# Optimization experiments

Hardware: AMD Instinct MI355X
Metric: run time of the kernel (lower is better)

## Reference

```python
import jax, jax.numpy as jnp
import numpy as np

SQRT_QKV_DIM = 8.0  # sqrt(qkv_dim=64)


def setup_inputs() -> dict:
    key = jax.random.key(0)
    ks = jax.random.split(key, 8)
    B, H, T, M, d, hid = 4, 16, 512, 512, 64, 16
    return {
        "q": jax.random.normal(ks[0], (B, H, T, d), dtype=jnp.float32),
        "k": jax.random.normal(ks[1], (B, H, M, d), dtype=jnp.float32),
        "v": jax.random.normal(ks[2], (B, H, M, d), dtype=jnp.float32),
        "D_TM": jax.random.uniform(ks[3], (B, T, M), dtype=jnp.float32),
        "mix1_weight": jax.random.uniform(ks[4], (H, 2, hid), minval=-0.7071, maxval=0.7071, dtype=jnp.float32),
        "mix1_bias": jax.random.uniform(ks[5], (H, hid), minval=-0.7071, maxval=0.7071, dtype=jnp.float32),
        "mix2_weight": jax.random.uniform(ks[6], (H, hid, 1), minval=-0.25, maxval=0.25, dtype=jnp.float32),
        "mix2_bias": jax.random.uniform(ks[7], (H, 1), minval=-0.25, maxval=0.25, dtype=jnp.float32),
    }


def reference(q, k, v, D_TM, mix1_weight, mix1_bias, mix2_weight, mix2_bias):
    B, H, T, d = q.shape
    Mc = k.shape[2]
    # scaled dot-product score: (B,H,T,M)
    dot_score = jnp.einsum("bhtd,bhmd->bhtm", q, k) / SQRT_QKV_DIM
    # per-head 2->hidden->1 MLP mixing dot score and distance bias.
    # Avoid explicit stack: linear layer over the 2 score channels expands as
    # dot*W1[:,0,:] + D*W1[:,1,:].  ms1: (B,H,T,M,hid)
    w1_dot = mix1_weight[:, 0, :][None, :, None, None, :]   # (1,H,1,1,hid)
    w1_dist = mix1_weight[:, 1, :][None, :, None, None, :]
    ms1 = (dot_score[..., None] * w1_dot
           + D_TM[:, None, :, :, None] * w1_dist
           + mix1_bias[None, :, None, None, :])
    ms1 = jax.nn.relu(ms1)
    # hidden -> 1: mixed_scores (B,H,T,M)
    mixed = jnp.einsum("bhtmc,hc->bhtm", ms1, mix2_weight[:, :, 0])
    mixed = mixed + mix2_bias[:, 0][None, :, None, None]
    weights = jax.nn.softmax(mixed, axis=3)
    out = jnp.einsum("bhtm,bhmd->bhtd", weights, v)   # (B,H,T,d)
    return out.transpose(0, 2, 1, 3).reshape(B, T, H * d)
```

## Files before the change

### kernel.cpp

```cpp
#include <hip/hip_runtime.h>
#include <stdint.h>

typedef __attribute__((ext_vector_type(8))) short short8;
typedef __attribute__((ext_vector_type(4))) float floatx4;

#define MFMA(a, b, c) __builtin_amdgcn_mfma_f32_16x16x32_bf16(a, b, c, 0, 0, 0)

union Frag { uint32_t u[4]; short8 s; };

__device__ __forceinline__ void packsplit(float a, float b, uint32_t& hi, uint32_t& lo) {
    uint32_t ua = __float_as_uint(a), ub = __float_as_uint(b);
    uint32_t ha = ua & 0xFFFF0000u, hb = ub & 0xFFFF0000u;
    float ra = a - __uint_as_float(ha);
    float rb = b - __uint_as_float(hb);
    hi = (ha >> 16) | hb;
    lo = (__float_as_uint(ra) >> 16) | (__float_as_uint(rb) & 0xFFFF0000u);
}

__device__ __forceinline__ float fexp2(float x) {
#if __has_builtin(__builtin_amdgcn_exp2f)
    return __builtin_amdgcn_exp2f(x);
#else
    return exp2f(x);
#endif
}

#define PHIo 9216
#define PLOo 11520

__global__ __launch_bounds__(256, 2)
void msmha_mfma(const float* __restrict__ qg, const float* __restrict__ kg,
                const float* __restrict__ vg, const float* __restrict__ Dg,
                const float* __restrict__ m1w, const float* __restrict__ m1b,
                const float* __restrict__ m2w, const float* __restrict__ m2b,
                float* __restrict__ outg) {
    __shared__ __align__(16) uint32_t sm[13824];
    __shared__ __align__(16) float4 wlds[16];

    const int tid  = threadIdx.x;
    const int w    = tid >> 6;
    const int lane = tid & 63;
    const int col  = lane & 15;
    const int quad = lane >> 4;

    const int bid = blockIdx.x;
    const int wgT = bid & 7;
    const int bh  = bid >> 3;
    const int h   = bh & 15;
    const int b   = bh >> 4;
    const int t0g = wgT * 64;

    const size_t base = (size_t)bh * 512 * 64;
    const float LOG2E = 1.4426950408889634f;

    if (tid < 16) {
        const float w1d = m1w[h * 32 + tid];
        const float w1s = m1w[h * 32 + 16 + tid];
        const float b1  = m1b[h * 16 + tid];
        const float w2  = m2w[h * 16 + tid];
        wlds[tid] = make_float4(w1d * (0.125f * LOG2E), w1s * LOG2E, b1 * LOG2E, 0.5f * w2);
    }

    float sA = 0.f, sB = 0.f, sC = 0.f;
#pragma unroll 1
    for (int c = 0; c < 16; ++c) {
        const float w2 = m2w[h * 16 + c];
        sA = fmaf(w2, m1w[h * 32 + c], sA);
        sB = fmaf(w2, m1w[h * 32 + 16 + c], sB);
        sC = fmaf(w2, m1b[h * 16 + c], sC);
    }
    const float Ac = sA * (0.0625f * LOG2E);
    const float Bc = sB * (0.5f * LOG2E);
    const float Cc = fmaf(0.5f, sC, m2b[h]) * LOG2E;

    Frag qh[2], ql[2];
    {
        const float* qrow = qg + base + (size_t)(t0g + w * 16 + col) * 64;
#pragma unroll
        for (int ks = 0; ks < 2; ++ks) {
            const float4 f0 = *(const float4*)(qrow + ks * 32 + quad * 8);
            const float4 f1 = *(const float4*)(qrow + ks * 32 + quad * 8 + 4);
            packsplit(f0.x, f0.y, qh[ks].u[0], ql[ks].u[0]);
            packsplit(f0.z, f0.w, qh[ks].u[1], ql[ks].u[1]);
            packsplit(f1.x, f1.y, qh[ks].u[2], ql[ks].u[2]);
            packsplit(f1.z, f1.w, qh[ks].u[3], ql[ks].u[3]);
        }
    }

    floatx4 accA[32];
    const float* Dbase = Dg + ((size_t)b * 512 + t0g + w * 16 + col) * 512 + quad * 4;

    const int ml0 = tid >> 4;
    const int k4  = tid & 15;
    float4 kreg[4];
    auto kload = [&](int mc) {
#pragma unroll
        for (int it = 0; it < 4; ++it)
            kreg[it] = *(const float4*)(kg + base + (size_t)(mc * 64 + ml0 + it * 16) * 64 + k4 * 4);
    };
    auto kwrite = [&](int p) {
        uint32_t* KH = sm + p * 4608;
        uint32_t* KL = KH + 2304;
#pragma unroll
        for (int it = 0; it < 4; ++it) {
            uint32_t h0, l0, h1, l1;
            packsplit(kreg[it].x, kreg[it].y, h0, l0);
            packsplit(kreg[it].z, kreg[it].w, h1, l1);
            const int ml = ml0 + it * 16;
            *(uint2*)(KH + ml * 36 + 2 * k4) = make_uint2(h0, h1);
            *(uint2*)(KL + ml * 36 + 2 * k4) = make_uint2(l0, l1);
        }
    };

    kload(0);
    kwrite(0);
    __syncthreads();

#pragma unroll
    for (int mc = 0; mc < 8; ++mc) {
        const int p = mc & 1;
        if (mc < 7) kload(mc + 1);

        float4 dv[4];
#pragma unroll
        for (int mt = 0; mt < 4; ++mt)
            dv[mt] = *(const float4*)(Dbase + mc * 64 + mt * 16);

        const uint32_t* KH = sm + p * 4608;
        const uint32_t* KL = KH + 2304;
        floatx4 sc[4];
#pragma unroll
        for (int mt = 0; mt < 4; ++mt) {
            floatx4 acc = {0.f, 0.f, 0.f, 0.f};
#pragma unroll
            for (int ks = 0; ks < 2; ++ks) {
                const int ro = (mt * 16 + col) * 36 + 16 * ks + 4 * quad;
                Frag ah, al;
                ah.s = *(const short8*)(KH + ro);
                al.s = *(const short8*)(KL + ro);
                acc = MFMA(ah.s, qh[ks].s, acc);
                acc = MFMA(ah.s, ql[ks].s, acc);
                acc = MFMA(al.s, qh[ks].s, acc);
            }
            sc[mt] = acc;
        }

        float dvf[16];
#pragma unroll
        for (int mt = 0; mt < 4; ++mt) {
            dvf[mt * 4 + 0] = dv[mt].x; dvf[mt * 4 + 1] = dv[mt].y;
            dvf[mt * 4 + 2] = dv[mt].z; dvf[mt * 4 + 3] = dv[mt].w;
        }
        float mix[16];
#pragma unroll
        for (int e = 0; e < 16; ++e) mix[e] = fmaf(dvf[e], Bc, Cc);
#pragma unroll 4
        for (int c = 0; c < 16; ++c) {
            const float4 wv = wlds[c];
#pragma unroll
            for (int mt = 0; mt < 4; ++mt)
#pragma unroll
                for (int r = 0; r < 4; ++r) {
                    const float hh = fmaf(sc[mt][r], wv.x, fmaf(dvf[mt * 4 + r], wv.y, wv.z));
                    mix[mt * 4 + r] = fmaf(fabsf(hh), wv.w, mix[mt * 4 + r]);
                }
        }
#pragma unroll
        for (int mt = 0; mt < 4; ++mt)
#pragma unroll
            for (int r = 0; r < 4; ++r)
                accA[mc * 4 + mt][r] = fmaf(sc[mt][r], Ac, mix[mt * 4 + r]);

        if (mc < 7) kwrite(p ^ 1);
        __syncthreads();
    }

    const int dgrp = tid & 15, m4 = tid >> 4;
    const int rotV = 8 * (dgrp & 3);
    float4 vreg[4];
    auto vload = [&](int mc) {
#pragma unroll
        for (int i = 0; i < 4; ++i)
            vreg[i] = *(const float4*)(vg + base + (size_t)(mc * 64 + 4 * m4 + i) * 64 + dgrp * 4);
    };
    auto vwrite = [&](int p) {
        uint32_t* VH = sm + p * 4608;
        uint32_t* VL = VH + 2304;
        const float a0[4] = {vreg[0].x, vreg[0].y, vreg[0].z, vreg[0].w};
        const float a1[4] = {vreg[1].x, vreg[1].y, vreg[1].z, vreg[1].w};
        const float a2[4] = {vreg[2].x, vreg[2].y, vreg[2].z, vreg[2].w};
        const float a3[4] = {vreg[3].x, vreg[3].y, vreg[3].z, vreg[3].w};
        const int cp = (2 * m4 + rotV) & 31;
#pragma unroll
        for (int jj = 0; jj < 4; ++jj) {
            uint32_t h0, l0, h1, l1;
            packsplit(a0[jj], a1[jj], h0, l0);
            packsplit(a2[jj], a3[jj], h1, l1);
            const int d = 4 * dgrp + jj;
            *(uint2*)(VH + d * 36 + cp) = make_uint2(h0, h1);
            *(uint2*)(VL + d * 36 + cp) = make_uint2(l0, l1);
        }
    };

    vload(0);

    float mx = -3.4e38f;
#pragma unroll
    for (int i = 0; i < 32; ++i)
#pragma unroll
        for (int r = 0; r < 4; ++r) mx = fmaxf(mx, accA[i][r]);
    mx = fmaxf(mx, __shfl_xor(mx, 16, 64));
    mx = fmaxf(mx, __shfl_xor(mx, 32, 64));
    float sum = 0.f;
#pragma unroll
    for (int i = 0; i < 32; ++i)
#pragma unroll
        for (int r = 0; r < 4; ++r) {
            const float e = fexp2(accA[i][r] - mx);
            accA[i][r] = e;
            sum += e;
        }
    sum += __shfl_xor(sum, 16, 64);
    sum += __shfl_xor(sum, 32, 64);
    const float rv = 1.f / sum;
    float rinvT[4];
#pragma unroll
    for (int r = 0; r < 4; ++r)
        rinvT[r] = __shfl(rv, quad * 4 + r, 64);

    vwrite(0);
    __syncthreads();

    floatx4 oacc[4];
#pragma unroll
    for (int dt = 0; dt < 4; ++dt) oacc[dt] = floatx4{0.f, 0.f, 0.f, 0.f};

    const int prow = (w * 16 + col) * 36;
    const int rotR = 8 * (col >> 2);

#pragma unroll
    for (int mc = 0; mc < 8; ++mc) {
        const int p = mc & 1;
        if (mc < 7) vload(mc + 1);

#pragma unroll
        for (int mt = 0; mt < 4; ++mt) {
            const floatx4 pv = accA[mc * 4 + mt];
            uint32_t h0, l0, h1, l1;
            packsplit(pv[0], pv[1], h0, l0);
            packsplit(pv[2], pv[3], h1, l1);
            *(uint2*)(sm + PHIo + prow + mt * 8 + 2 * quad) = make_uint2(h0, h1);
            *(uint2*)(sm + PLOo + prow + mt * 8 + 2 * quad) = make_uint2(l0, l1);
        }

        const uint32_t* VH = sm + p * 4608;
        const uint32_t* VL = VH + 2304;
#pragma unroll
        for (int ks = 0; ks < 2; ++ks) {
            const int po = prow + 16 * ks + 4 * quad;
            Frag pah, pal;
            pah.s = *(const short8*)(sm + PHIo + po);
            pal.s = *(const short8*)(sm + PLOo + po);
            const int cb = ((16 * ks + 4 * quad) + rotR) & 31;
#pragma unroll
            for (int dt = 0; dt < 4; ++dt) {
                const int vo = (dt * 16 + col) * 36 + cb;
                Frag bh, bl;
                bh.s = *(const short8*)(VH + vo);
                bl.s = *(const short8*)(VL + vo);
                oacc[dt] = MFMA(pah.s, bh.s, oacc[dt]);
                oacc[dt] = MFMA(pah.s, bl.s, oacc[dt]);
                oacc[dt] = MFMA(pal.s, bh.s, oacc[dt]);
            }
        }

        if (mc < 7) vwrite(p ^ 1);
        __syncthreads();
    }

    const size_t obase = ((size_t)b * 512 + t0g + w * 16 + quad * 4) * 1024 + h * 64 + col;
#pragma unroll
    for (int dt = 0; dt < 4; ++dt)
#pragma unroll
        for (int r = 0; r < 4; ++r)
            outg[obase + (size_t)r * 1024 + dt * 16] = oacc[dt][r] * rinvT[r];
}

extern "C" void kernel_launch(void* const* d_in, const int* in_sizes, int n_in,
                              void* d_out, int out_size, void* d_ws, size_t ws_size,
                              hipStream_t stream) {
    const float* q   = (const float*)d_in[0];
    const float* k   = (const float*)d_in[1];
    const float* v   = (const float*)d_in[2];
    const float* dtm = (const float*)d_in[3];
    const float* m1w = (const float*)d_in[4];
    const float* m1b = (const float*)d_in[5];
    const float* m2w = (const float*)d_in[6];
    const float* m2b = (const float*)d_in[7];
    float* out = (float*)d_out;

    dim3 grid(4 * 16 * 8);
    dim3 block(256);
    msmha_mfma<<<grid, block, 0, stream>>>(q, k, v, dtm, m1w, m1b, m2w, m2b, out);
}
```

Measured before the change: 134.5 us.

## Restructure to flash-style online softmax with split-KV across two wave groups

Replaces the two-phase kernel, which stored all scores in 128 registers before a separate softmax and PV pass, with a flash-attention style loop using an online running max and sum. The block doubles to 512 threads, split into two groups that each handle half of the key/value sequence, and the groups merge their partial results through shared memory at the end. This cuts register pressure so occupancy can rise, and adds parallelism per query tile. In exchange it drops the double-buffered K/V prefetch, adds extra barriers per chunk, and pays for rescaling and the final merge.

```diff
diff --git a/kernel.cpp b/kernel.cpp
--- a/kernel.cpp
+++ b/kernel.cpp
@@ -25,23 +25,24 @@
 #endif
 }
 
-#define PHIo 9216
-#define PLOo 11520
-
-__global__ __launch_bounds__(256, 2)
-void msmha_mfma(const float* __restrict__ qg, const float* __restrict__ kg,
-                const float* __restrict__ vg, const float* __restrict__ Dg,
-                const float* __restrict__ m1w, const float* __restrict__ m1b,
-                const float* __restrict__ m2w, const float* __restrict__ m2b,
-                float* __restrict__ outg) {
-    __shared__ __align__(16) uint32_t sm[13824];
+
+__global__ __launch_bounds__(512, 4)
+void msmha_flash(const float* __restrict__ qg, const float* __restrict__ kg,
+                 const float* __restrict__ vg, const float* __restrict__ Dg,
+                 const float* __restrict__ m1w, const float* __restrict__ m1b,
+                 const float* __restrict__ m2w, const float* __restrict__ m2b,
+                 float* __restrict__ outg) {
+    __shared__ __align__(16) uint32_t sm[18432];
     __shared__ __align__(16) float4 wlds[16];
 
-    const int tid  = threadIdx.x;
-    const int w    = tid >> 6;
-    const int lane = tid & 63;
-    const int col  = lane & 15;
-    const int quad = lane >> 4;
+    const int tid   = threadIdx.x;
+    const int w     = tid >> 6;
+    const int group = w >> 2;
+    const int gw    = w & 3;
+    const int lane  = tid & 63;
+    const int col   = lane & 15;
+    const int quad  = lane >> 4;
+    const int gtid  = tid & 255;
 
     const int bid = blockIdx.x;
     const int wgT = bid & 7;
@@ -75,7 +76,7 @@
 
     Frag qh[2], ql[2];
     {
-        const float* qrow = qg + base + (size_t)(t0g + w * 16 + col) * 64;
+        const float* qrow = qg + base + (size_t)(t0g + gw * 16 + col) * 64;
 #pragma unroll
         for (int ks = 0; ks < 2; ++ks) {
             const float4 f0 = *(const float4*)(qrow + ks * 32 + quad * 8);
@@ -87,47 +88,60 @@
         }
     }
 
-    floatx4 accA[32];
-    const float* Dbase = Dg + ((size_t)b * 512 + t0g + w * 16 + col) * 512 + quad * 4;
-
-    const int ml0 = tid >> 4;
-    const int k4  = tid & 15;
-    float4 kreg[4];
-    auto kload = [&](int mc) {
+    const int ml0  = gtid >> 4;
+    const int k4   = gtid & 15;
+    const int dgrp = gtid & 15;
+    const int m4   = gtid >> 4;
+    const int cpV  = (2 * m4 + 8 * ((dgrp >> 1) & 3)) & 31;
+    const int rsel = col >> 3;
+
+    const int gb = group * 9216;
+    uint32_t* KH = sm + gb;
+    uint32_t* KL = sm + gb + 2304;
+    uint32_t* VH = sm + gb + 4608;
+    uint32_t* VL = sm + gb + 6912;
+
+    const int moff = group * 256;
+    const float* kc = kg + base + (size_t)moff * 64;
+    const float* vc = vg + base + (size_t)moff * 64;
+    const float* Dc = Dg + ((size_t)b * 512 + t0g + gw * 16 + col) * 512 + moff + quad * 4;
+
+    float run_m = -3.0e38f, run_l = 0.f;
+    floatx4 oacc[4];
+#pragma unroll
+    for (int dt = 0; dt < 4; ++dt) oacc[dt] = floatx4{0.f, 0.f, 0.f, 0.f};
+
+#pragma unroll 1
+    for (int mc = 0; mc < 4; ++mc) {
+        const float* kp = kc + (size_t)mc * 64 * 64;
+        const float* vp = vc + (size_t)mc * 64 * 64;
+
+        float4 kr[4], vr[4];
 #pragma unroll
         for (int it = 0; it < 4; ++it)
-            kreg[it] = *(const float4*)(kg + base + (size_t)(mc * 64 + ml0 + it * 16) * 64 + k4 * 4);
-    };
-    auto kwrite = [&](int p) {
-        uint32_t* KH = sm + p * 4608;
-        uint32_t* KL = KH + 2304;
+            kr[it] = *(const float4*)(kp + (size_t)(ml0 + it * 16) * 64 + k4 * 4);
+#pragma unroll
+        for (int i = 0; i < 4; ++i)
+            vr[i] = *(const float4*)(vp + (size_t)(4 * m4 + i) * 64 + dgrp * 4);
+        float dvf[16];
+#pragma unroll
+        for (int mt = 0; mt < 4; ++mt) {
+            const float4 dd = *(const float4*)(Dc + mc * 64 + mt * 16);
+            dvf[mt * 4 + 0] = dd.x; dvf[mt * 4 + 1] = dd.y;
+            dvf[mt * 4 + 2] = dd.z; dvf[mt * 4 + 3] = dd.w;
+        }
+
 #pragma unroll
         for (int it = 0; it < 4; ++it) {
             uint32_t h0, l0, h1, l1;
-            packsplit(kreg[it].x, kreg[it].y, h0, l0);
-            packsplit(kreg[it].z, kreg[it].w, h1, l1);
+            packsplit(kr[it].x, kr[it].y, h0, l0);
+            packsplit(kr[it].z, kr[it].w, h1, l1);
             const int ml = ml0 + it * 16;
             *(uint2*)(KH + ml * 36 + 2 * k4) = make_uint2(h0, h1);
             *(uint2*)(KL + ml * 36 + 2 * k4) = make_uint2(l0, l1);
         }
-    };
-
-    kload(0);
-    kwrite(0);
-    __syncthreads();
-
-#pragma unroll
-    for (int mc = 0; mc < 8; ++mc) {
-        const int p = mc & 1;
-        if (mc < 7) kload(mc + 1);
-
-        float4 dv[4];
-#pragma unroll
-        for (int mt = 0; mt < 4; ++mt)
-            dv[mt] = *(const float4*)(Dbase + mc * 64 + mt * 16);
-
-        const uint32_t* KH = sm + p * 4608;
-        const uint32_t* KL = KH + 2304;
+        __syncthreads();
+
         floatx4 sc[4];
 #pragma unroll
         for (int mt = 0; mt < 4; ++mt) {
@@ -145,12 +159,6 @@
             sc[mt] = acc;
         }
 
-        float dvf[16];
-#pragma unroll
-        for (int mt = 0; mt < 4; ++mt) {
-            dvf[mt * 4 + 0] = dv[mt].x; dvf[mt * 4 + 1] = dv[mt].y;
-            dvf[mt * 4 + 2] = dv[mt].z; dvf[mt * 4 + 3] = dv[mt].w;
-        }
         float mix[16];
 #pragma unroll
         for (int e = 0; e < 16; ++e) mix[e] = fmaf(dvf[e], Bc, Cc);
@@ -169,121 +177,120 @@
         for (int mt = 0; mt < 4; ++mt)
 #pragma unroll
             for (int r = 0; r < 4; ++r)
-                accA[mc * 4 + mt][r] = fmaf(sc[mt][r], Ac, mix[mt * 4 + r]);
-
-        if (mc < 7) kwrite(p ^ 1);
-        __syncthreads();
-    }
-
-    const int dgrp = tid & 15, m4 = tid >> 4;
-    const int rotV = 8 * (dgrp & 3);
-    float4 vreg[4];
-    auto vload = [&](int mc) {
-#pragma unroll
-        for (int i = 0; i < 4; ++i)
-            vreg[i] = *(const float4*)(vg + base + (size_t)(mc * 64 + 4 * m4 + i) * 64 + dgrp * 4);
-    };
-    auto vwrite = [&](int p) {
-        uint32_t* VH = sm + p * 4608;
-        uint32_t* VL = VH + 2304;
-        const float a0[4] = {vreg[0].x, vreg[0].y, vreg[0].z, vreg[0].w};
-        const float a1[4] = {vreg[1].x, vreg[1].y, vreg[1].z, vreg[1].w};
-        const float a2[4] = {vreg[2].x, vreg[2].y, vreg[2].z, vreg[2].w};
-        const float a3[4] = {vreg[3].x, vreg[3].y, vreg[3].z, vreg[3].w};
-        const int cp = (2 * m4 + rotV) & 31;
+                sc[mt][r] = fmaf(sc[mt][r], Ac, mix[mt * 4 + r]);
+
 #pragma unroll
         for (int jj = 0; jj < 4; ++jj) {
             uint32_t h0, l0, h1, l1;
-            packsplit(a0[jj], a1[jj], h0, l0);
-            packsplit(a2[jj], a3[jj], h1, l1);
+            packsplit(((const float*)&vr[0])[jj], ((const float*)&vr[1])[jj], h0, l0);
+            packsplit(((const float*)&vr[2])[jj], ((const float*)&vr[3])[jj], h1, l1);
             const int d = 4 * dgrp + jj;
-            *(uint2*)(VH + d * 36 + cp) = make_uint2(h0, h1);
-            *(uint2*)(VL + d * 36 + cp) = make_uint2(l0, l1);
-        }
-    };
-
-    vload(0);
-
-    float mx = -3.4e38f;
-#pragma unroll
-    for (int i = 0; i < 32; ++i)
-#pragma unroll
-        for (int r = 0; r < 4; ++r) mx = fmaxf(mx, accA[i][r]);
-    mx = fmaxf(mx, __shfl_xor(mx, 16, 64));
-    mx = fmaxf(mx, __shfl_xor(mx, 32, 64));
-    float sum = 0.f;
-#pragma unroll
-    for (int i = 0; i < 32; ++i)
-#pragma unroll
-        for (int r = 0; r < 4; ++r) {
-            const float e = fexp2(accA[i][r] - mx);
-            accA[i][r] = e;
-            sum += e;
-        }
-    sum += __shfl_xor(sum, 16, 64);
-    sum += __shfl_xor(sum, 32, 64);
-    const float rv = 1.f / sum;
-    float rinvT[4];
-#pragma unroll
-    for (int r = 0; r < 4; ++r)
-        rinvT[r] = __shfl(rv, quad * 4 + r, 64);
-
-    vwrite(0);
-    __syncthreads();
-
-    floatx4 oacc[4];
-#pragma unroll
-    for (int dt = 0; dt < 4; ++dt) oacc[dt] = floatx4{0.f, 0.f, 0.f, 0.f};
-
-    const int prow = (w * 16 + col) * 36;
-    const int rotR = 8 * (col >> 2);
-
-#pragma unroll
-    for (int mc = 0; mc < 8; ++mc) {
-        const int p = mc & 1;
-        if (mc < 7) vload(mc + 1);
-
+            *(uint2*)(VH + d * 36 + cpV) = make_uint2(h0, h1);
+            *(uint2*)(VL + d * 36 + cpV) = make_uint2(l0, l1);
+        }
+
+        float cmx = -3.0e38f;
+#pragma unroll
+        for (int mt = 0; mt < 4; ++mt)
+#pragma unroll
+            for (int r = 0; r < 4; ++r) cmx = fmaxf(cmx, sc[mt][r]);
+        cmx = fmaxf(cmx, __shfl_xor(cmx, 16, 64));
+        cmx = fmaxf(cmx, __shfl_xor(cmx, 32, 64));
+        const float nm    = fmaxf(run_m, cmx);
+        const float scale = fexp2(run_m - nm);
+        float csum = 0.f;
+#pragma unroll
+        for (int mt = 0; mt < 4; ++mt)
+#pragma unroll
+            for (int r = 0; r < 4; ++r) {
+                const float p = fexp2(sc[mt][r] - nm);
+                sc[mt][r] = p;
+                csum += p;
+            }
+        csum += __shfl_xor(csum, 16, 64);
+        csum += __shfl_xor(csum, 32, 64);
+        run_l = fmaf(run_l, scale, csum);
+        run_m = nm;
+        float sOT[4];
+#pragma unroll
+        for (int r = 0; r < 4; ++r) sOT[r] = __shfl(scale, quad * 4 + r, 64);
+#pragma unroll
+        for (int dt = 0; dt < 4; ++dt)
+#pragma unroll
+            for (int r = 0; r < 4; ++r) oacc[dt][r] *= sOT[r];
+
+        __syncthreads();
+
+        const int prow = (gw * 16 + col) * 36;
 #pragma unroll
         for (int mt = 0; mt < 4; ++mt) {
-            const floatx4 pv = accA[mc * 4 + mt];
             uint32_t h0, l0, h1, l1;
-            packsplit(pv[0], pv[1], h0, l0);
-            packsplit(pv[2], pv[3], h1, l1);
-            *(uint2*)(sm + PHIo + prow + mt * 8 + 2 * quad) = make_uint2(h0, h1);
-            *(uint2*)(sm + PLOo + prow + mt * 8 + 2 * quad) = make_uint2(l0, l1);
-        }
-
-        const uint32_t* VH = sm + p * 4608;
-        const uint32_t* VL = VH + 2304;
+            packsplit(sc[mt][0], sc[mt][1], h0, l0);
+            packsplit(sc[mt][2], sc[mt][3], h1, l1);
+            *(uint2*)(KH + prow + mt * 8 + 2 * quad) = make_uint2(h0, h1);
+            *(uint2*)(KL + prow + mt * 8 + 2 * quad) = make_uint2(l0, l1);
+        }
+
 #pragma unroll
         for (int ks = 0; ks < 2; ++ks) {
             const int po = prow + 16 * ks + 4 * quad;
             Frag pah, pal;
-            pah.s = *(const short8*)(sm + PHIo + po);
-            pal.s = *(const short8*)(sm + PLOo + po);
-            const int cb = ((16 * ks + 4 * quad) + rotR) & 31;
+            pah.s = *(const short8*)(KH + po);
+            pal.s = *(const short8*)(KL + po);
 #pragma unroll
             for (int dt = 0; dt < 4; ++dt) {
-                const int vo = (dt * 16 + col) * 36 + cb;
-                Frag bh, bl;
-                bh.s = *(const short8*)(VH + vo);
-                bl.s = *(const short8*)(VL + vo);
-                oacc[dt] = MFMA(pah.s, bh.s, oacc[dt]);
-                oacc[dt] = MFMA(pah.s, bl.s, oacc[dt]);
-                oacc[dt] = MFMA(pal.s, bh.s, oacc[dt]);
+                const int cbd = ((16 * ks + 4 * quad) + 8 * ((2 * dt + rsel) & 3)) & 31;
+                const int vo = (dt * 16 + col) * 36 + cbd;
+                Frag bhv, blv;
+                bhv.s = *(const short8*)(VH + vo);
+                blv.s = *(const short8*)(VL + vo);
+                oacc[dt] = MFMA(pah.s, bhv.s, oacc[dt]);
+                oacc[dt] = MFMA(pah.s, blv.s, oacc[dt]);
+                oacc[dt] = MFMA(pal.s, bhv.s, oacc[dt]);
             }
         }
-
-        if (mc < 7) vwrite(p ^ 1);
         __syncthreads();
     }
 
-    const size_t obase = ((size_t)b * 512 + t0g + w * 16 + quad * 4) * 1024 + h * 64 + col;
-#pragma unroll
-    for (int dt = 0; dt < 4; ++dt)
-#pragma unroll
-        for (int r = 0; r < 4; ++r)
-            outg[obase + (size_t)r * 1024 + dt * 16] = oacc[dt][r] * rinvT[r];
+    float* smf = (float*)sm;
+    if (group == 1) {
+        if (quad == 0) {
+            smf[13376 + gw * 16 + col] = run_m;
+            smf[13440 + gw * 16 + col] = run_l;
+        }
+        const int t = gw * 16 + quad * 4;
+#pragma unroll
+        for (int dt = 0; dt < 4; ++dt)
+#pragma unroll
+            for (int r = 0; r < 4; ++r)
+                smf[9216 + (t + r) * 65 + dt * 16 + col] = oacc[dt][r];
+    }
+    __syncthreads();
+    if (group == 0) {
+        const float m1c = smf[13376 + gw * 16 + col];
+        const float l1c = smf[13440 + gw * 16 + col];
+        const float M   = fmaxf(run_m, m1c);
+        const float s0  = fexp2(run_m - M);
+        const float s1  = fexp2(m1c - M);
+        const float rdn = 1.f / fmaf(run_l, s0, l1c * s1);
+        float s0T[4], s1T[4], rdT[4];
+#pragma unroll
+        for (int r = 0; r < 4; ++r) {
+            s0T[r] = __shfl(s0, quad * 4 + r, 64);
+            s1T[r] = __shfl(s1, quad * 4 + r, 64);
+            rdT[r] = __shfl(rdn, quad * 4 + r, 64);
+        }
+        const int t = gw * 16 + quad * 4;
+        const size_t obase = ((size_t)b * 512 + t0g + t) * 1024 + h * 64 + col;
+#pragma unroll
+        for (int dt = 0; dt < 4; ++dt)
+#pragma unroll
+            for (int r = 0; r < 4; ++r) {
+                const float o1 = smf[9216 + (t + r) * 65 + dt * 16 + col];
+                outg[obase + (size_t)r * 1024 + dt * 16] =
+                    fmaf(oacc[dt][r], s0T[r], o1 * s1T[r]) * rdT[r];
+            }
+    }
 }
 
 extern "C" void kernel_launch(void* const* d_in, const int* in_sizes, int n_in,
@@ -300,6 +307,6 @@
     float* out = (float*)d_out;
 
     dim3 grid(4 * 16 * 8);
-    dim3 block(256);
-    msmha_mfma<<<grid, block, 0, stream>>>(q, k, v, dtm, m1w, m1b, m2w, m2b, out);
+    dim3 block(512);
+    msmha_flash<<<grid, block, 0, stream>>>(q, k, v, dtm, m1w, m1b, m2w, m2b, out);
 }
```

Measured after the change: 132.4 us. No clear change (-1.5%).
